# Optimization experiments

Hardware: AMD Instinct MI355X
Metric: run time of the kernel (lower is better)

The kernel has to match this reference:

```python
import jax, jax.numpy as jnp
import numpy as np


def setup_inputs() -> dict:
    key = jax.random.key(0)
    ks = jax.random.split(key, 6)
    B, IN, H, OUT = 4096, 1024, 2048, 256
    s1 = 1.0 / np.sqrt(IN)
    s2 = 1.0 / np.sqrt(H)
    return {
        "x": jax.random.normal(ks[0], (B, IN), dtype=jnp.float32),
        "W1": jax.random.uniform(ks[1], (H, IN), jnp.float32, -s1, s1),
        "b1": jax.random.uniform(ks[2], (H,), jnp.float32, -s1, s1),
        "W2": jax.random.uniform(ks[3], (OUT, H), jnp.float32, -s2, s2),
        "b2": jax.random.uniform(ks[4], (OUT,), jnp.float32, -s2, s2),
        "tau_mem": jnp.float32(10.0),
        "tau_syn": jnp.float32(5.0),
        "v_thresh": jnp.float32(1.0),
        "v_reset": jnp.float32(0.0),
        "v_mem0": jnp.zeros((B, H), jnp.float32),
        "i_syn0": jnp.zeros((B, H), jnp.float32),
        "time_steps": 32,
    }


def reference(x, W1, b1, W2, b2, tau_mem, tau_syn, v_thresh, v_reset, v_mem0, i_syn0, time_steps):
    dt = jnp.float32(1.0)
    # fc1(x)/time_steps is identical every step in the original loop; compute once.
    cur = (x @ W1.T + b1) / jnp.float32(time_steps)  # [B, H]

    def step(carry, _):
        v, i = carry
        i = i - (dt / tau_syn) * i + cur
        v = v - (dt / tau_mem) * v + i
        s = (v >= v_thresh).astype(x.dtype)
        v = v * (1.0 - s) + v_reset * s
        return (v, i), s

    (_, _), spikes = jax.lax.scan(step, (v_mem0, i_syn0), None, length=time_steps)
    total_spikes = spikes.sum(axis=0)  # [B, H]
    output = total_spikes @ W2.T + b2  # [B, OUT]
    return output, total_spikes
```

## Files before the change

### kernel.cpp

```cpp
#include <hip/hip_runtime.h>
#include <hip/hip_bf16.h>
#include <stdint.h>

typedef __attribute__((ext_vector_type(8))) short bf16x8;
typedef __attribute__((ext_vector_type(4))) float f32x4;

__device__ __forceinline__ float vmulf(float a, float b) {
    float d; asm volatile("v_mul_f32 %0, %1, %2" : "=v"(d) : "v"(a), "v"(b)); return d;
}
__device__ __forceinline__ float vaddf(float a, float b) {
    float d; asm volatile("v_add_f32 %0, %1, %2" : "=v"(d) : "v"(a), "v"(b)); return d;
}
__device__ __forceinline__ float vsubf(float a, float b) {
    float d; asm volatile("v_sub_f32 %0, %1, %2" : "=v"(d) : "v"(a), "v"(b)); return d;
}

__device__ __forceinline__ short bf16h(float v) {
    __hip_bfloat16 h = __float2bfloat16(v);
    return *(short*)&h;
}
__device__ __forceinline__ float bf16f(short s) {
    return __uint_as_float(((unsigned int)(unsigned short)s) << 16);
}
__device__ __forceinline__ void split2(float v, short& h, short& m) {
    h = bf16h(v);
    m = bf16h(__fsub_rn(v, bf16f(h)));
}

__device__ __forceinline__ float decode_scalar(const void* p, float dflt) {
    float f = *(const float*)p;
    if (!(f == f) || fabsf(f) > 1.0e6f) return dflt;
    return f;
}
__device__ __forceinline__ int decode_ts(const void* p) {
    int w = *(const int*)p;
    if (w >= 1 && w <= 100000) return w;
    return 32;
}

#define LDA 36

__global__ __launch_bounds__(256) void k1_panel_gemm(
    const float* __restrict__ X,
    const float* __restrict__ W1,
    float* __restrict__ P0,
    float* __restrict__ P1,
    int M, int N, int K, int KC)
{
    __shared__ float As[128][LDA];
    __shared__ float Bs[128][LDA];

    const int t  = threadIdx.x;
    const int tx = t & 15;
    const int ty = t >> 4;
    const int m0 = blockIdx.x * 128;
    const int n0 = blockIdx.y * 128;
    const int kz = blockIdx.z * KC;
    float* __restrict__ Pout = blockIdx.z ? P1 : P0;

    float p[8][8] = {};

    for (int k0 = kz; k0 < kz + KC; k0 += 32) {
        #pragma unroll
        for (int cc = 0; cc < 4; ++cc) {
            const int li  = cc * 256 + t;
            const int row = li >> 3;
            const int q   = li & 7;
            *(float4*)&As[row][q * 4] =
                *(const float4*)&X[(size_t)(m0 + row) * K + k0 + q * 4];
            *(float4*)&Bs[row][q * 4] =
                *(const float4*)&W1[(size_t)(n0 + row) * K + k0 + q * 4];
        }
        __syncthreads();

        #pragma unroll
        for (int g = 0; g < 8; ++g) {
            float4 af[8], bf[8];
            #pragma unroll
            for (int i = 0; i < 8; ++i)
                af[i] = *(const float4*)&As[ty + 16 * i][g * 4];
            #pragma unroll
            for (int j = 0; j < 8; ++j)
                bf[j] = *(const float4*)&Bs[tx + 16 * j][g * 4];
            #pragma unroll
            for (int kk = 0; kk < 4; ++kk) {
                #pragma unroll
                for (int i = 0; i < 8; ++i) {
                    const float a = ((const float*)&af[i])[kk];
                    #pragma unroll
                    for (int j = 0; j < 8; ++j)
                        p[i][j] = __builtin_fmaf(a, ((const float*)&bf[j])[kk], p[i][j]);
                }
            }
        }
        __syncthreads();
    }

    #pragma unroll
    for (int i = 0; i < 8; ++i) {
        const size_t rowb = (size_t)(m0 + ty + 16 * i) * N;
        #pragma unroll
        for (int j = 0; j < 8; ++j)
            Pout[rowb + n0 + tx + 16 * j] = p[i][j];
    }
}

__global__ __launch_bounds__(256) void k1_combine_scan(
    const float* __restrict__ P0,
    const float* __restrict__ P1,
    const float* __restrict__ b1,
    const void* tau_mem_p, const void* tau_syn_p,
    const void* v_thresh_p, const void* v_reset_p, const void* ts_p,
    float* __restrict__ spikes, int N, int total4)
{
    const int idx4 = blockIdx.x * 256 + threadIdx.x;
    if (idx4 >= total4) return;

    const float tau_m = decode_scalar(tau_mem_p, 10.0f);
    const float tau_s = decode_scalar(tau_syn_p, 5.0f);
    const float vth   = decode_scalar(v_thresh_p, 1.0f);
    const float vrs   = decode_scalar(v_reset_p, 0.0f);
    const int   ts    = decode_ts(ts_p);
    const float rs    = 1.0f / tau_s;
    const float rm    = 1.0f / tau_m;
    const float ivts  = 1.0f / (float)ts;

    const float4 a = ((const float4*)P0)[idx4];
    const float4 b = ((const float4*)P1)[idx4];
    const int col0 = (idx4 * 4) % N;
    const float4 bb = *(const float4*)&b1[col0];

    float cur[4], iv[4], vv[4], cnt[4];
    const float av[4] = {a.x, a.y, a.z, a.w};
    const float bv[4] = {b.x, b.y, b.z, b.w};
    const float bbv[4] = {bb.x, bb.y, bb.z, bb.w};
    #pragma unroll
    for (int e = 0; e < 4; ++e) {
        const float c = vaddf(av[e], bv[e]);
        cur[e] = vmulf(vaddf(c, bbv[e]), ivts);
        iv[e] = 0.0f; vv[e] = 0.0f; cnt[e] = 0.0f;
    }
    for (int tt = 0; tt < ts; ++tt) {
        #pragma unroll
        for (int e = 0; e < 4; ++e) {
            iv[e] = vaddf(vsubf(iv[e], vmulf(rs, iv[e])), cur[e]);
            vv[e] = vaddf(vsubf(vv[e], vmulf(rm, vv[e])), iv[e]);
            const bool s = (vv[e] >= vth);
            cnt[e] += s ? 1.0f : 0.0f;
            vv[e]   = s ? vrs : vv[e];
        }
    }
    ((float4*)spikes)[idx4] = make_float4(cnt[0], cnt[1], cnt[2], cnt[3]);
}

__global__ __launch_bounds__(256) void k1_f32chain_snn(
    const float* __restrict__ X, const float* __restrict__ W1,
    const float* __restrict__ b1,
    const void* tau_mem_p, const void* tau_syn_p,
    const void* v_thresh_p, const void* v_reset_p, const void* ts_p,
    float* __restrict__ spikes, int M, int N, int K, int f0)
{
    __shared__ float As[128][LDA];
    __shared__ float Bs[128][LDA];

    const int t  = threadIdx.x;
    const int tx = t & 15;
    const int ty = t >> 4;
    const int m0 = blockIdx.x * 128;
    const int n0 = blockIdx.y * 128;

    float c[8][8] = {};
    float p[8][8] = {};

    for (int k0 = 0; k0 < K; k0 += 32) {
        #pragma unroll
        for (int cc = 0; cc < 4; ++cc) {
            const int li  = cc * 256 + t;
            const int row = li >> 3;
            const int q   = li & 7;
            *(float4*)&As[row][q * 4] =
                *(const float4*)&X[(size_t)(m0 + row) * K + k0 + q * 4];
            *(float4*)&Bs[row][q * 4] =
                *(const float4*)&W1[(size_t)(n0 + row) * K + k0 + q * 4];
        }
        __syncthreads();
        #pragma unroll
        for (int g = 0; g < 8; ++g) {
            float4 af[8], bf[8];
            #pragma unroll
            for (int i = 0; i < 8; ++i)
                af[i] = *(const float4*)&As[ty + 16 * i][g * 4];
            #pragma unroll
            for (int j = 0; j < 8; ++j)
                bf[j] = *(const float4*)&Bs[tx + 16 * j][g * 4];
            #pragma unroll
            for (int kk = 0; kk < 4; ++kk) {
                #pragma unroll
                for (int i = 0; i < 8; ++i) {
                    const float a = ((const float*)&af[i])[kk];
                    #pragma unroll
                    for (int j = 0; j < 8; ++j)
                        p[i][j] = __builtin_fmaf(a, ((const float*)&bf[j])[kk], p[i][j]);
                }
            }
        }
        __syncthreads();
        const int ke = k0 + 32;
        if (ke == f0 || ke == K) {
            #pragma unroll
            for (int i = 0; i < 8; ++i)
                #pragma unroll
                for (int j = 0; j < 8; ++j) {
                    c[i][j] = vaddf(c[i][j], p[i][j]);
                    p[i][j] = 0.0f;
                }
        }
    }

    const float tau_m = decode_scalar(tau_mem_p, 10.0f);
    const float tau_s = decode_scalar(tau_syn_p, 5.0f);
    const float vth   = decode_scalar(v_thresh_p, 1.0f);
    const float vrs   = decode_scalar(v_reset_p, 0.0f);
    const int   ts    = decode_ts(ts_p);
    const float rs    = 1.0f / tau_s;
    const float rm    = 1.0f / tau_m;
    const float ivts  = 1.0f / (float)ts;

    #pragma unroll
    for (int j = 0; j < 8; ++j) {
        const int col    = n0 + tx + 16 * j;
        const float bias = b1[col];
        float cur[8], iv[8], vv[8], cnt[8];
        #pragma unroll
        for (int i = 0; i < 8; ++i) {
            cur[i] = vmulf(vaddf(c[i][j], bias), ivts);
            iv[i] = 0.0f; vv[i] = 0.0f; cnt[i] = 0.0f;
        }
        for (int tt = 0; tt < ts; ++tt) {
            #pragma unroll
            for (int i = 0; i < 8; ++i) {
                iv[i] = vaddf(vsubf(iv[i], vmulf(rs, iv[i])), cur[i]);
                vv[i] = vaddf(vsubf(vv[i], vmulf(rm, vv[i])), iv[i]);
                const bool s = (vv[i] >= vth);
                cnt[i] += s ? 1.0f : 0.0f;
                vv[i]   = s ? vrs : vv[i];
            }
        }
        #pragma unroll
        for (int i = 0; i < 8; ++i)
            spikes[(size_t)(m0 + ty + 16 * i) * N + col] = cnt[i];
    }
}

__global__ __launch_bounds__(256) void k2_partial(
    const float* __restrict__ S, const float* __restrict__ W2,
    float* __restrict__ Pt,
    int M, int N2, int K2, int KC2)
{
    __shared__ __align__(16) short Sa[64 * 32];
    __shared__ __align__(16) short Bh[64 * 32];
    __shared__ __align__(16) short Bm[64 * 32];

    const int t    = threadIdx.x;
    const int l    = t & 63;
    const int w    = t >> 6;
    const int quad = l >> 4;
    const int r    = l & 15;
    const int wm   = w & 1;
    const int wn   = w >> 1;

    const int m0 = blockIdx.x * 64;
    const int n0 = blockIdx.y * 64;
    const int kz = blockIdx.z * KC2;
    float* __restrict__ outp = Pt + (size_t)blockIdx.z * M * N2;

    f32x4 acc[2][2] = {};

    for (int k0 = kz; k0 < kz + KC2; k0 += 32) {
        #pragma unroll
        for (int cc = 0; cc < 2; ++cc) {
            const int li  = cc * 256 + t;
            const int row = li >> 3;
            const int q   = li & 7;
            const float4 vs = *(const float4*)&S[(size_t)(m0 + row) * K2 + k0 + q * 4];
            *(short4*)&Sa[row * 32 + q * 4] =
                make_short4(bf16h(vs.x), bf16h(vs.y), bf16h(vs.z), bf16h(vs.w));
            const float4 vb = *(const float4*)&W2[(size_t)(n0 + row) * K2 + k0 + q * 4];
            short h[4], m_[4];
            split2(vb.x, h[0], m_[0]); split2(vb.y, h[1], m_[1]);
            split2(vb.z, h[2], m_[2]); split2(vb.w, h[3], m_[3]);
            *(short4*)&Bh[row * 32 + q * 4] = make_short4(h[0], h[1], h[2], h[3]);
            *(short4*)&Bm[row * 32 + q * 4] = make_short4(m_[0], m_[1], m_[2], m_[3]);
        }
        __syncthreads();

        bf16x8 af[2], bh[2], bm[2];
        #pragma unroll
        for (int i = 0; i < 2; ++i) {
            af[i] = *(const bf16x8*)&Sa[(wm * 32 + i * 16 + r) * 32 + quad * 8];
            bh[i] = *(const bf16x8*)&Bh[(wn * 32 + i * 16 + r) * 32 + quad * 8];
            bm[i] = *(const bf16x8*)&Bm[(wn * 32 + i * 16 + r) * 32 + quad * 8];
        }
        #pragma unroll
        for (int i = 0; i < 2; ++i)
            #pragma unroll
            for (int j = 0; j < 2; ++j) {
                acc[i][j] = __builtin_amdgcn_mfma_f32_16x16x32_bf16(af[i], bh[j], acc[i][j], 0, 0, 0);
                acc[i][j] = __builtin_amdgcn_mfma_f32_16x16x32_bf16(af[i], bm[j], acc[i][j], 0, 0, 0);
            }
        __syncthreads();
    }

    #pragma unroll
    for (int j = 0; j < 2; ++j) {
        const int col = n0 + wn * 32 + j * 16 + r;
        #pragma unroll
        for (int i = 0; i < 2; ++i) {
            const int rowb = m0 + wm * 32 + i * 16 + quad * 4;
            #pragma unroll
            for (int e = 0; e < 4; ++e)
                outp[(size_t)(rowb + e) * N2 + col] = acc[i][j][e];
        }
    }
}

__global__ __launch_bounds__(256) void k2_combine(
    const float* __restrict__ Pt, const float* __restrict__ b2,
    float* __restrict__ out, int N2, int total4, size_t stride4)
{
    const int idx4 = blockIdx.x * 256 + threadIdx.x;
    if (idx4 >= total4) return;
    float4 s = ((const float4*)Pt)[idx4];
    #pragma unroll
    for (int z = 1; z < 4; ++z) {
        const float4 v = ((const float4*)Pt)[stride4 * z + idx4];
        s.x += v.x; s.y += v.y; s.z += v.z; s.w += v.w;
    }
    const float4 bb = *(const float4*)&b2[(idx4 * 4) % N2];
    s.x += bb.x; s.y += bb.y; s.z += bb.z; s.w += bb.w;
    ((float4*)out)[idx4] = s;
}

__global__ __launch_bounds__(256) void k2_gemm(
    const float* __restrict__ S, const float* __restrict__ W2,
    const float* __restrict__ b2, float* __restrict__ out,
    int M, int N2, int K2)
{
    __shared__ __align__(16) short Sa[64 * 32];
    __shared__ __align__(16) short Bh[64 * 32];
    __shared__ __align__(16) short Bm[64 * 32];

    const int t    = threadIdx.x;
    const int l    = t & 63;
    const int w    = t >> 6;
    const int quad = l >> 4;
    const int r    = l & 15;
    const int wm   = w & 1;
    const int wn   = w >> 1;

    const int m0 = blockIdx.x * 64;
    const int n0 = blockIdx.y * 64;

    f32x4 acc[2][2] = {};

    for (int k0 = 0; k0 < K2; k0 += 32) {
        #pragma unroll
        for (int cc = 0; cc < 2; ++cc) {
            const int li  = cc * 256 + t;
            const int row = li >> 3;
            const int q   = li & 7;
            const float4 vs = *(const float4*)&S[(size_t)(m0 + row) * K2 + k0 + q * 4];
            *(short4*)&Sa[row * 32 + q * 4] =
                make_short4(bf16h(vs.x), bf16h(vs.y), bf16h(vs.z), bf16h(vs.w));
            const float4 vb = *(const float4*)&W2[(size_t)(n0 + row) * K2 + k0 + q * 4];
            short h[4], m_[4];
            split2(vb.x, h[0], m_[0]); split2(vb.y, h[1], m_[1]);
            split2(vb.z, h[2], m_[2]); split2(vb.w, h[3], m_[3]);
            *(short4*)&Bh[row * 32 + q * 4] = make_short4(h[0], h[1], h[2], h[3]);
            *(short4*)&Bm[row * 32 + q * 4] = make_short4(m_[0], m_[1], m_[2], m_[3]);
        }
        __syncthreads();

        bf16x8 af[2], bh[2], bm[2];
        #pragma unroll
        for (int i = 0; i < 2; ++i) {
            af[i] = *(const bf16x8*)&Sa[(wm * 32 + i * 16 + r) * 32 + quad * 8];
            bh[i] = *(const bf16x8*)&Bh[(wn * 32 + i * 16 + r) * 32 + quad * 8];
            bm[i] = *(const bf16x8*)&Bm[(wn * 32 + i * 16 + r) * 32 + quad * 8];
        }
        #pragma unroll
        for (int i = 0; i < 2; ++i)
            #pragma unroll
            for (int j = 0; j < 2; ++j) {
                acc[i][j] = __builtin_amdgcn_mfma_f32_16x16x32_bf16(af[i], bh[j], acc[i][j], 0, 0, 0);
                acc[i][j] = __builtin_amdgcn_mfma_f32_16x16x32_bf16(af[i], bm[j], acc[i][j], 0, 0, 0);
            }
        __syncthreads();
    }

    #pragma unroll
    for (int j = 0; j < 2; ++j) {
        const int col = n0 + wn * 32 + j * 16 + r;
        const float bias = b2[col];
        #pragma unroll
        for (int i = 0; i < 2; ++i) {
            const int rowb = m0 + wm * 32 + i * 16 + quad * 4;
            #pragma unroll
            for (int e = 0; e < 4; ++e)
                out[(size_t)(rowb + e) * N2 + col] = __fadd_rn(acc[i][j][e], bias);
        }
    }
}

extern "C" void kernel_launch(void* const* d_in, const int* in_sizes, int n_in,
                              void* d_out, int out_size, void* d_ws, size_t ws_size,
                              hipStream_t stream) {
    (void)n_in; (void)out_size;

    const float* X  = (const float*)d_in[0];
    const float* W1 = (const float*)d_in[1];
    const float* b1 = (const float*)d_in[2];
    const float* W2 = (const float*)d_in[3];
    const float* b2 = (const float*)d_in[4];
    const void* tau_mem = d_in[5];
    const void* tau_syn = d_in[6];
    const void* vth     = d_in[7];
    const void* vrs     = d_in[8];
    const void* ts      = d_in[11];

    const int H   = in_sizes[2];
    const int IN  = in_sizes[1] / H;
    const int OUT = in_sizes[4];
    const int B   = in_sizes[0] / IN;

    float* out    = (float*)d_out;
    float* spikes = out + (size_t)B * OUT;

    const int KC = 512;
    const size_t panel_bytes = (size_t)B * H * sizeof(float);
    const bool ws_ok = (IN == 2 * KC) && (ws_size >= panel_bytes) &&
                       ((uintptr_t)d_ws % 16 == 0);

    if (ws_ok) {
        float* P1 = (float*)d_ws;
        dim3 g1(B / 128, H / 128, 2);
        k1_panel_gemm<<<g1, 256, 0, stream>>>(X, W1, spikes, P1, B, H, IN, KC);

        const int total4 = (B * H) / 4;
        k1_combine_scan<<<(total4 + 255) / 256, 256, 0, stream>>>(
            spikes, P1, b1, tau_mem, tau_syn, vth, vrs, ts, spikes, H, total4);
    } else {
        dim3 g1(B / 128, H / 128);
        k1_f32chain_snn<<<g1, 256, 0, stream>>>(X, W1, b1, tau_mem, tau_syn, vth, vrs, ts,
                                                spikes, B, H, IN, KC);
    }

    const int KC2 = 512;
    const size_t k2_part_bytes = 4 * (size_t)B * OUT * sizeof(float);
    if (ws_ok && H == 4 * KC2 && ws_size >= k2_part_bytes) {
        float* Pt = (float*)d_ws;
        dim3 g2(B / 64, OUT / 64, 4);
        k2_partial<<<g2, 256, 0, stream>>>(spikes, W2, Pt, B, OUT, H, KC2);
        const int total4 = (B * OUT) / 4;
        k2_combine<<<(total4 + 255) / 256, 256, 0, stream>>>(
            Pt, b2, out, OUT, total4, (size_t)B * OUT / 4);
    } else {
        dim3 g2(B / 64, OUT / 64);
        k2_gemm<<<g2, 256, 0, stream>>>(spikes, W2, b2, out, B, OUT, H);
    }
}
```

Before: 417.1 us.

## Double-buffer GEMM tiles with direct global-to-LDS loads and XOR swizzle

Rewrites the fp32 panel GEMM main loop to use global_load_lds (direct global-to-LDS DMA) into double-buffered 16-wide K chunks. The next chunk is prefetched while the current one is computed, with one barrier per chunk. An XOR swizzle on the column index replaces the padded LDA layout to avoid bank conflicts. This aims to hide global load latency and cut register staging, at the cost of smaller K chunks per barrier and stricter alignment and layout assumptions.

Measured after the change: 416.3 us, median of 2. No clear change (-0.2%).

```diff
diff --git a/kernel.cpp b/kernel.cpp
--- a/kernel.cpp
+++ b/kernel.cpp
@@ -36,6 +36,12 @@
     int w = *(const int*)p;
     if (w >= 1 && w <= 100000) return w;
     return 32;
+}
+
+__device__ __forceinline__ void gl16(const float* g, float* l) {
+    __builtin_amdgcn_global_load_lds(
+        (const __attribute__((address_space(1))) unsigned int*)g,
+        (__attribute__((address_space(3))) unsigned int*)l, 16, 0, 0);
 }
 
 #define LDA 36
@@ -47,8 +53,8 @@
     float* __restrict__ P1,
     int M, int N, int K, int KC)
 {
-    __shared__ float As[128][LDA];
-    __shared__ float Bs[128][LDA];
+    __shared__ __align__(16) float As[2][128][16];
+    __shared__ __align__(16) float Bs[2][128][16];
 
     const int t  = threadIdx.x;
     const int tx = t & 15;
@@ -60,40 +66,56 @@
 
     float p[8][8] = {};
 
-    for (int k0 = kz; k0 < kz + KC; k0 += 32) {
-        #pragma unroll
-        for (int cc = 0; cc < 4; ++cc) {
-            const int li  = cc * 256 + t;
-            const int row = li >> 3;
-            const int q   = li & 7;
-            *(float4*)&As[row][q * 4] =
-                *(const float4*)&X[(size_t)(m0 + row) * K + k0 + q * 4];
-            *(float4*)&Bs[row][q * 4] =
-                *(const float4*)&W1[(size_t)(n0 + row) * K + k0 + q * 4];
-        }
-        __syncthreads();
-
-        #pragma unroll
-        for (int g = 0; g < 8; ++g) {
-            float4 af[8], bf[8];
-            #pragma unroll
-            for (int i = 0; i < 8; ++i)
-                af[i] = *(const float4*)&As[ty + 16 * i][g * 4];
+    const int w     = t >> 6;
+    const int l     = t & 63;
+    const int r0    = 32 * w + (l >> 2);
+    const int r1    = r0 + 16;
+    const int selem = ((l & 3) ^ ((l >> 3) & 3)) << 2;
+    const int oa0 = (m0 + r0) * K + selem;
+    const int oa1 = (m0 + r1) * K + selem;
+    const int ob0 = (n0 + r0) * K + selem;
+    const int ob1 = (n0 + r1) * K + selem;
+
+    gl16(X  + oa0 + kz, &As[0][32 * w][0]);
+    gl16(X  + oa1 + kz, &As[0][32 * w + 16][0]);
+    gl16(W1 + ob0 + kz, &Bs[0][32 * w][0]);
+    gl16(W1 + ob1 + kz, &Bs[0][32 * w + 16][0]);
+
+    const int cax = (ty >> 1) & 3;
+    const int cbx = (tx >> 1) & 3;
+
+    const int nch = KC >> 4;
+    for (int c = 0; c < nch; ++c) {
+        __syncthreads();
+        const int d = c & 1;
+        if (c + 1 < nch) {
+            const int kn = kz + ((c + 1) << 4);
+            const int dn = d ^ 1;
+            gl16(X  + oa0 + kn, &As[dn][32 * w][0]);
+            gl16(X  + oa1 + kn, &As[dn][32 * w + 16][0]);
+            gl16(W1 + ob0 + kn, &Bs[dn][32 * w][0]);
+            gl16(W1 + ob1 + kn, &Bs[dn][32 * w + 16][0]);
+        }
+        #pragma unroll
+        for (int g = 0; g < 4; ++g) {
+            float4 bfv[8];
+            const int cb = (g ^ cbx) << 2;
             #pragma unroll
             for (int j = 0; j < 8; ++j)
-                bf[j] = *(const float4*)&Bs[tx + 16 * j][g * 4];
-            #pragma unroll
-            for (int kk = 0; kk < 4; ++kk) {
+                bfv[j] = *(const float4*)&Bs[d][tx + 16 * j][cb];
+            const int ca = (g ^ cax) << 2;
+            #pragma unroll
+            for (int i = 0; i < 8; ++i) {
+                const float4 af = *(const float4*)&As[d][ty + 16 * i][ca];
                 #pragma unroll
-                for (int i = 0; i < 8; ++i) {
-                    const float a = ((const float*)&af[i])[kk];
+                for (int kk = 0; kk < 4; ++kk) {
+                    const float a = ((const float*)&af)[kk];
                     #pragma unroll
                     for (int j = 0; j < 8; ++j)
-                        p[i][j] = __builtin_fmaf(a, ((const float*)&bf[j])[kk], p[i][j]);
+                        p[i][j] = __builtin_fmaf(a, ((const float*)&bfv[j])[kk], p[i][j]);
                 }
             }
         }
-        __syncthreads();
     }
 
     #pragma unroll
```
